# Kernel tuning notes

Measured on AMD Instinct MI355X. Metric: run time of the kernel, lower is better.

The kernel has to match this reference:

```python
import jax, jax.numpy as jnp
import numpy as np

INPUT_SIZE = 1024
HIDDEN_SIZE = 1024
NUM_LAYERS = 5
B, T = 64, 512


def setup_inputs() -> dict:
    key = jax.random.key(0)
    ks = jax.random.split(key, 12)
    scale_in = 1.0 / np.sqrt(INPUT_SIZE)
    scale_h = 1.0 / np.sqrt(HIDDEN_SIZE)
    return {
        "x": jax.random.normal(ks[0], (B, T, INPUT_SIZE), dtype=jnp.float32),
        "s0": jnp.zeros((B, HIDDEN_SIZE), dtype=jnp.float32),
        "w_h": jax.random.normal(ks[1], (INPUT_SIZE, HIDDEN_SIZE), dtype=jnp.float32) * scale_in,
        "w_t": jax.random.normal(ks[2], (INPUT_SIZE, HIDDEN_SIZE), dtype=jnp.float32) * scale_in,
        "w_c": jax.random.normal(ks[3], (INPUT_SIZE, HIDDEN_SIZE), dtype=jnp.float32) * scale_in,
        "r_hw": jax.random.normal(ks[4], (NUM_LAYERS, HIDDEN_SIZE, HIDDEN_SIZE), dtype=jnp.float32) * scale_h,
        "r_tw": jax.random.normal(ks[5], (NUM_LAYERS, HIDDEN_SIZE, HIDDEN_SIZE), dtype=jnp.float32) * scale_h,
        "r_cw": jax.random.normal(ks[6], (NUM_LAYERS, HIDDEN_SIZE, HIDDEN_SIZE), dtype=jnp.float32) * scale_h,
        "r_hb": jnp.zeros((NUM_LAYERS, HIDDEN_SIZE), dtype=jnp.float32),
        "r_tb": jnp.full((NUM_LAYERS, HIDDEN_SIZE), -1.0, dtype=jnp.float32),  # transform bias init
        "r_cb": jnp.zeros((NUM_LAYERS, HIDDEN_SIZE), dtype=jnp.float32),
    }


def reference(x, s0, w_h, w_t, w_c, r_hw, r_tw, r_cw, r_hb, r_tb, r_cb):
    # x: [B, T, D_in]; s0: [B, H]. dropout=0 -> dropout layers are identity.
    L = r_hw.shape[0]

    def step(s, x_t):
        # Input projections only feed layer 0 (l == 0 in the torch loop).
        whx = x_t @ w_h  # [B, H]
        wtx = x_t @ w_t
        wcx = x_t @ w_c
        for l in range(L):  # small fixed recurrence depth
            h_in = s @ r_hw[l] + r_hb[l]
            t_in = s @ r_tw[l] + r_tb[l]
            c_in = s @ r_cw[l] + r_cb[l]
            if l == 0:
                h_in = h_in + whx
                t_in = t_in + wtx
                c_in = c_in + wcx
            h = jnp.tanh(h_in)
            t = jax.nn.sigmoid(t_in)
            c = jax.nn.sigmoid(c_in)
            s = h * t + s * c
        return s, s

    xs = jnp.swapaxes(x, 0, 1)  # [T, B, D_in] for scan over time
    s_final, ys = jax.lax.scan(step, s0, xs)
    outputs = jnp.swapaxes(ys, 0, 1)  # [B, T, H]
    return outputs, s_final
```

## Files before the change

### kernel.cpp

```cpp
#include <hip/hip_runtime.h>

typedef _Float16 f16;
typedef f16  f16x8 __attribute__((ext_vector_type(8)));
typedef float f32x4 __attribute__((ext_vector_type(4)));
typedef unsigned int u32;
typedef unsigned long long u64;

#define NBLK   256
#define TPB    512
#define TSTEPS 512
#define NL     5
#define HDIM   1024
#define NROUND (TSTEPS*NL)
#define WSLOT  6
#define LDS_RED_OFF 147456
#define SMEM_BYTES  (147456 + 4096)

__device__ __forceinline__ float fsigmoid(float v){ return 1.0f/(1.0f + __expf(-v)); }
__device__ __forceinline__ float ftanh(float v){ return 1.0f - 2.0f/(__expf(2.0f*v) + 1.0f); }

__device__ __forceinline__ size_t frag_off_bytes(int row, int col){
    const int mt = row >> 4, pp = row & 15;
    const int kh = col >> 9, kk = (col >> 5) & 15, g8 = (col >> 3) & 3, i = col & 7;
    return (size_t)(((kh*4 + mt)*16 + kk)*1024 + (g8*16 + pp)*16 + i*2);
}

__global__ void cvt_x_kernel(const float* __restrict__ x, f16* __restrict__ xT){
    const size_t idx = (size_t)blockIdx.x*blockDim.x + threadIdx.x;
    const size_t e = idx*8;
    const int k  = (int)(e & 1023);
    const int tt = (int)((e >> 10) & 511);
    const int b  = (int)(e >> 19);
    const float4 v0 = *(const float4*)(x + e);
    const float4 v1 = *(const float4*)(x + e + 4);
    f16x8 o;
    o[0]=(f16)v0.x; o[1]=(f16)v0.y; o[2]=(f16)v0.z; o[3]=(f16)v0.w;
    o[4]=(f16)v1.x; o[5]=(f16)v1.y; o[6]=(f16)v1.z; o[7]=(f16)v1.w;
    char* dst = (char*)xT + (size_t)tt*131072 + frag_off_bytes(b, k);
    *(f16x8*)dst = o;
}

#define LOADA(i) asm volatile("global_load_dwordx4 %0, %1, off sc0 sc1" : "=v"(a##i) : "v"(ap + (i)*1024))

template<bool USE_XT>
__global__ __launch_bounds__(TPB, 2)
void rhn_persistent(const float* __restrict__ x,
                    const f16*  __restrict__ xT,
                    const float* __restrict__ s0,
                    const float* __restrict__ w_h, const float* __restrict__ w_t, const float* __restrict__ w_c,
                    const float* __restrict__ r_hw, const float* __restrict__ r_tw, const float* __restrict__ r_cw,
                    const float* __restrict__ r_hb, const float* __restrict__ r_tb, const float* __restrict__ r_cb,
                    f16* __restrict__ sb0, f16* __restrict__ sb1,
                    u32* __restrict__ flags,
                    float* __restrict__ out)
{
    extern __shared__ char smem[];
    f16*   lw  = (f16*)smem;
    f32x4* red = (f32x4*)(smem + LDS_RED_OFF);

    const int tid = threadIdx.x;
    const int ln  = tid & 63;
    const int wid = tid >> 6;
    const int mt  = wid & 3;
    const int kh  = wid >> 2;
    const int c   = blockIdx.x;
    const int g   = ln >> 4;
    const int p   = ln & 15;
    const int pe  = (p < 12) ? p : 11;
    const int gsw = (g + (pe >> 1)) & 3;

    for (int s = 0; s < WSLOT; ++s) {
        for (int mu = 0; mu < 3; ++mu) {
            const float* W;
            if (s < NL) W = (mu==0 ? r_hw : (mu==1 ? r_tw : r_cw)) + (size_t)s*HDIM*HDIM;
            else        W = (mu==0 ? w_h  : (mu==1 ? w_t  : w_c));
            for (int k = tid; k < HDIM; k += TPB) {
                const float4 v = *(const float4*)(W + (size_t)k*HDIM + 4*c);
                const int kk = k >> 5, gg = (k >> 3) & 3, ii = k & 7;
                #pragma unroll
                for (int w = 0; w < 4; ++w) {
                    const int pe2 = mu*4 + w;
                    const int gs  = (gg + (pe2 >> 1)) & 3;
                    const float val = (w==0) ? v.x : (w==1) ? v.y : (w==2) ? v.z : v.w;
                    lw[((s*32 + kk)*12 + pe2)*32 + gs*8 + ii] = (f16)val;
                }
            }
        }
    }

    const int R    = ln >> 2;
    const int jj   = ln & 3;
    const int jcol = 4*c + jj;
    const int bat  = mt*16 + R;
    const size_t sfoff = frag_off_bytes(bat, jcol & ~1);
    float s_cur = 0.f;
    float bh[NL], bt[NL], bc[NL];
    if (kh == 0) {
        s_cur = s0[(size_t)bat*HDIM + jcol];
        #pragma unroll
        for (int l = 0; l < NL; ++l) {
            bh[l] = r_hb[l*HDIM + jcol];
            bt[l] = r_tb[l*HDIM + jcol];
            bc[l] = r_cb[l*HDIM + jcol];
        }
        union { f16 h; unsigned short u; } cv; cv.h = (f16)s_cur;
        u32 mybits = cv.u;
        u32 otherbits = (u32)(unsigned short)__shfl_xor((int)mybits, 1);
        if ((jj & 1) == 0) {
            u32 packed = mybits | (otherbits << 16);
            u32* dst = (u32*)((char*)sb0 + sfoff);
            __hip_atomic_store(dst, packed, __ATOMIC_RELAXED, __HIP_MEMORY_SCOPE_AGENT);
        }
        asm volatile("s_waitcnt vmcnt(0)" ::: "memory");
    }
    __syncthreads();
    if (tid == 0)
        __hip_atomic_store(&flags[c], 1u, __ATOMIC_RELAXED, __HIP_MEMORY_SCOPE_AGENT);

    const f16* sbufs[2] = { sb0, sb1 };
    int t = 0, l = 0;
    unsigned guard = 0;

    for (int r = 0; r < NROUND; ++r) {
        const u32 tgt = (u32)(r + 1);
        if (mt == 0 && guard < (1u<<22)) {
            const u64* fp = (const u64*)&flags[kh*128 + 2*ln];
            for (;;) {
                u64 ff = __hip_atomic_load(fp, __ATOMIC_RELAXED, __HIP_MEMORY_SCOPE_AGENT);
                if (__all((u32)ff >= tgt && (u32)(ff >> 32) >= tgt)) break;
                if (++guard >= (1u<<22)) break;
                __builtin_amdgcn_s_sleep(2);
            }
        }
        __syncthreads();

        const char* ap = (const char*)sbufs[r & 1] + (size_t)((kh*4 + mt)*16)*1024 + ln*16;
        f16x8 a0,a1,a2,a3,a4,a5,a6,a7,a8,a9,a10,a11,a12,a13,a14,a15;
        LOADA(0);  LOADA(1);  LOADA(2);  LOADA(3);
        LOADA(4);  LOADA(5);  LOADA(6);  LOADA(7);
        LOADA(8);  LOADA(9);  LOADA(10); LOADA(11);
        LOADA(12); LOADA(13); LOADA(14); LOADA(15);

        f32x4 acc = {0.f,0.f,0.f,0.f};
        const f16* bp = lw + ((l*32 + kh*16)*12 + pe)*32 + gsw*8;

        if (l == 0) {
            const f16* bp5 = lw + ((5*32 + kh*16)*12 + pe)*32 + gsw*8;
            if (USE_XT) {
                const f16* xp = xT + (size_t)t*65536 + (size_t)((kh*4 + mt)*16)*512 + ln*8;
                #pragma unroll
                for (int kk = 0; kk < 16; ++kk) {
                    f16x8 xa = *(const f16x8*)(xp + kk*512);
                    f16x8 b  = *(const f16x8*)(bp5 + kk*384);
                    acc = __builtin_amdgcn_mfma_f32_16x16x32_f16(xa, b, acc, 0, 0, 0);
                }
            } else {
                const int arow = mt*16 + p;
                const float* xp = x + ((size_t)arow*TSTEPS + t)*HDIM + kh*512 + g*8;
                #pragma unroll
                for (int kk = 0; kk < 16; ++kk) {
                    float4 v0 = *(const float4*)(xp + kk*32);
                    float4 v1 = *(const float4*)(xp + kk*32 + 4);
                    f16x8 xa;
                    xa[0]=(f16)v0.x; xa[1]=(f16)v0.y; xa[2]=(f16)v0.z; xa[3]=(f16)v0.w;
                    xa[4]=(f16)v1.x; xa[5]=(f16)v1.y; xa[6]=(f16)v1.z; xa[7]=(f16)v1.w;
                    f16x8 b = *(const f16x8*)(bp5 + kk*384);
                    acc = __builtin_amdgcn_mfma_f32_16x16x32_f16(xa, b, acc, 0, 0, 0);
                }
            }
        }

        asm volatile("s_waitcnt vmcnt(0)" ::: "memory");
        __builtin_amdgcn_sched_barrier(0);
        acc = __builtin_amdgcn_mfma_f32_16x16x32_f16(a0,  *(const f16x8*)(bp + 0*384),  acc, 0,0,0);
        acc = __builtin_amdgcn_mfma_f32_16x16x32_f16(a1,  *(const f16x8*)(bp + 1*384),  acc, 0,0,0);
        acc = __builtin_amdgcn_mfma_f32_16x16x32_f16(a2,  *(const f16x8*)(bp + 2*384),  acc, 0,0,0);
        acc = __builtin_amdgcn_mfma_f32_16x16x32_f16(a3,  *(const f16x8*)(bp + 3*384),  acc, 0,0,0);
        acc = __builtin_amdgcn_mfma_f32_16x16x32_f16(a4,  *(const f16x8*)(bp + 4*384),  acc, 0,0,0);
        acc = __builtin_amdgcn_mfma_f32_16x16x32_f16(a5,  *(const f16x8*)(bp + 5*384),  acc, 0,0,0);
        acc = __builtin_amdgcn_mfma_f32_16x16x32_f16(a6,  *(const f16x8*)(bp + 6*384),  acc, 0,0,0);
        acc = __builtin_amdgcn_mfma_f32_16x16x32_f16(a7,  *(const f16x8*)(bp + 7*384),  acc, 0,0,0);
        acc = __builtin_amdgcn_mfma_f32_16x16x32_f16(a8,  *(const f16x8*)(bp + 8*384),  acc, 0,0,0);
        acc = __builtin_amdgcn_mfma_f32_16x16x32_f16(a9,  *(const f16x8*)(bp + 9*384),  acc, 0,0,0);
        acc = __builtin_amdgcn_mfma_f32_16x16x32_f16(a10, *(const f16x8*)(bp + 10*384), acc, 0,0,0);
        acc = __builtin_amdgcn_mfma_f32_16x16x32_f16(a11, *(const f16x8*)(bp + 11*384), acc, 0,0,0);
        acc = __builtin_amdgcn_mfma_f32_16x16x32_f16(a12, *(const f16x8*)(bp + 12*384), acc, 0,0,0);
        acc = __builtin_amdgcn_mfma_f32_16x16x32_f16(a13, *(const f16x8*)(bp + 13*384), acc, 0,0,0);
        acc = __builtin_amdgcn_mfma_f32_16x16x32_f16(a14, *(const f16x8*)(bp + 14*384), acc, 0,0,0);
        acc = __builtin_amdgcn_mfma_f32_16x16x32_f16(a15, *(const f16x8*)(bp + 15*384), acc, 0,0,0);

        if (kh == 1) red[mt*64 + ln] = acc;
        __syncthreads();
        if (kh == 0) {
            acc += red[mt*64 + ln];
            const int sl = (R >> 2)*16 + jj;
            const int ri = R & 3;
            float hv, tv, cv;
            { float v0=__shfl(acc[0],sl),   v1=__shfl(acc[1],sl),   v2=__shfl(acc[2],sl),   v3=__shfl(acc[3],sl);
              hv = ri==0?v0: ri==1?v1: ri==2?v2: v3; }
            { float v0=__shfl(acc[0],sl+4), v1=__shfl(acc[1],sl+4), v2=__shfl(acc[2],sl+4), v3=__shfl(acc[3],sl+4);
              tv = ri==0?v0: ri==1?v1: ri==2?v2: v3; }
            { float v0=__shfl(acc[0],sl+8), v1=__shfl(acc[1],sl+8), v2=__shfl(acc[2],sl+8), v3=__shfl(acc[3],sl+8);
              cv = ri==0?v0: ri==1?v1: ri==2?v2: v3; }
            hv += bh[l]; tv += bt[l]; cv += bc[l];
            const float hh = ftanh(hv);
            const float tg = fsigmoid(tv);
            const float cg = fsigmoid(cv);
            const float s_new = hh*tg + s_cur*cg;
            s_cur = s_new;
            f16* sbn = (f16*)sbufs[(r + 1) & 1];
            union { f16 h; unsigned short u; } cv2; cv2.h = (f16)s_new;
            u32 mybits = cv2.u;
            u32 otherbits = (u32)(unsigned short)__shfl_xor((int)mybits, 1);
            if ((jj & 1) == 0) {
                u32 packed = mybits | (otherbits << 16);
                u32* dst = (u32*)((char*)sbn + sfoff);
                __hip_atomic_store(dst, packed, __ATOMIC_RELAXED, __HIP_MEMORY_SCOPE_AGENT);
            }
            if (l == NL-1) out[((size_t)bat*TSTEPS + t)*HDIM + jcol] = s_new;
            asm volatile("s_waitcnt vmcnt(0)" ::: "memory");
        }
        __syncthreads();
        if (tid == 0)
            __hip_atomic_store(&flags[c], (u32)(r + 2), __ATOMIC_RELAXED, __HIP_MEMORY_SCOPE_AGENT);

        if (++l == NL) { l = 0; ++t; }
    }
    if (kh == 0)
        out[(size_t)64*TSTEPS*HDIM + (size_t)bat*HDIM + jcol] = s_cur;
}

extern "C" void kernel_launch(void* const* d_in, const int* in_sizes, int n_in,
                              void* d_out, int out_size, void* d_ws, size_t ws_size,
                              hipStream_t stream)
{
    const float* x    = (const float*)d_in[0];
    const float* s0   = (const float*)d_in[1];
    const float* w_h  = (const float*)d_in[2];
    const float* w_t  = (const float*)d_in[3];
    const float* w_c  = (const float*)d_in[4];
    const float* r_hw = (const float*)d_in[5];
    const float* r_tw = (const float*)d_in[6];
    const float* r_cw = (const float*)d_in[7];
    const float* r_hb = (const float*)d_in[8];
    const float* r_tb = (const float*)d_in[9];
    const float* r_cb = (const float*)d_in[10];
    float* out = (float*)d_out;

    char* ws   = (char*)d_ws;
    u32*  flags = (u32*)ws;
    f16*  sb0  = (f16*)(ws + 4096);
    f16*  sb1  = (f16*)(ws + 4096 + 131072);
    f16*  xT   = (f16*)(ws + 4096 + 262144);
    const size_t need_xt = 4096 + 262144 + (size_t)TSTEPS*64*HDIM*2;
    const bool use_xt = (ws_size >= need_xt);

    hipMemsetAsync(flags, 0, 1024, stream);
    if (use_xt)
        cvt_x_kernel<<<dim3(16384), dim3(256), 0, stream>>>(x, xT);

    hipFuncSetAttribute((const void*)rhn_persistent<true>,
                        hipFuncAttributeMaxDynamicSharedMemorySize, SMEM_BYTES);
    hipFuncSetAttribute((const void*)rhn_persistent<false>,
                        hipFuncAttributeMaxDynamicSharedMemorySize, SMEM_BYTES);

    if (use_xt)
        rhn_persistent<true><<<dim3(NBLK), dim3(TPB), SMEM_BYTES, stream>>>(
            x, xT, s0, w_h, w_t, w_c, r_hw, r_tw, r_cw, r_hb, r_tb, r_cb,
            sb0, sb1, flags, out);
    else
        rhn_persistent<false><<<dim3(NBLK), dim3(TPB), SMEM_BYTES, stream>>>(
            x, xT, s0, w_h, w_t, w_c, r_hw, r_tw, r_cw, r_hb, r_tb, r_cb,
            sb0, sb1, flags, out);
}
```

Baseline: 17.30 ms.

## Halve block size so each wave owns full K and drop intra-block barriers

The persistent kernel goes from 512 to 256 threads per block. Each wave now covers the full 1024-wide reduction with two accumulators, so the LDS cross-wave reduction and its __syncthreads disappear. Every wave polls all 256 flags itself, and a shared atomic counter lets the fourth finishing wave publish the block's flag, replacing the block barriers around the flag wait and store. The cost is twice the register pressure for the A fragments, more polling traffic per block, and a longer serial MFMA chain per wave.

```diff
diff --git a/kernel.cpp b/kernel.cpp
--- a/kernel.cpp
+++ b/kernel.cpp
@@ -7,14 +7,20 @@
 typedef unsigned long long u64;
 
 #define NBLK   256
-#define TPB    512
+#define TPB    256
 #define TSTEPS 512
 #define NL     5
 #define HDIM   1024
 #define NROUND (TSTEPS*NL)
 #define WSLOT  6
-#define LDS_RED_OFF 147456
-#define SMEM_BYTES  (147456 + 4096)
+#define GMAX   (1u<<22)
+#define SMEM_BYTES  147456
+
+#define WS_FLAGS 0
+#define WS_SB0   4096
+#define WS_SB1   (4096 + 131072)
+#define WS_XT    (4096 + 262144)
+#define WS_NEED  ((size_t)(4096 + 262144) + (size_t)TSTEPS*64*HDIM*2)
 
 __device__ __forceinline__ float fsigmoid(float v){ return 1.0f/(1.0f + __expf(-v)); }
 __device__ __forceinline__ float ftanh(float v){ return 1.0f - 2.0f/(__expf(2.0f*v) + 1.0f); }
@@ -40,10 +46,10 @@
     *(f16x8*)dst = o;
 }
 
-#define LOADA(i) asm volatile("global_load_dwordx4 %0, %1, off sc0 sc1" : "=v"(a##i) : "v"(ap + (i)*1024))
+#define LOADA(v, base, i) asm volatile("global_load_dwordx4 %0, %1, off sc0 sc1" : "=v"(v) : "v"((base) + (i)*1024))
 
 template<bool USE_XT>
-__global__ __launch_bounds__(TPB, 2)
+__global__ __launch_bounds__(TPB, 1)
 void rhn_persistent(const float* __restrict__ x,
                     const f16*  __restrict__ xT,
                     const float* __restrict__ s0,
@@ -55,14 +61,12 @@
                     float* __restrict__ out)
 {
     extern __shared__ char smem[];
-    f16*   lw  = (f16*)smem;
-    f32x4* red = (f32x4*)(smem + LDS_RED_OFF);
+    f16* lw = (f16*)smem;
+    __shared__ u32 done;
 
     const int tid = threadIdx.x;
     const int ln  = tid & 63;
-    const int wid = tid >> 6;
-    const int mt  = wid & 3;
-    const int kh  = wid >> 2;
+    const int w   = tid >> 6;
     const int c   = blockIdx.x;
     const int g   = ln >> 4;
     const int p   = ln & 15;
@@ -78,31 +82,33 @@
                 const float4 v = *(const float4*)(W + (size_t)k*HDIM + 4*c);
                 const int kk = k >> 5, gg = (k >> 3) & 3, ii = k & 7;
                 #pragma unroll
-                for (int w = 0; w < 4; ++w) {
-                    const int pe2 = mu*4 + w;
+                for (int q = 0; q < 4; ++q) {
+                    const int pe2 = mu*4 + q;
                     const int gs  = (gg + (pe2 >> 1)) & 3;
-                    const float val = (w==0) ? v.x : (w==1) ? v.y : (w==2) ? v.z : v.w;
+                    const float val = (q==0) ? v.x : (q==1) ? v.y : (q==2) ? v.z : v.w;
                     lw[((s*32 + kk)*12 + pe2)*32 + gs*8 + ii] = (f16)val;
                 }
             }
         }
     }
+
+    if (tid == 0) done = 0;
+    __syncthreads();
 
     const int R    = ln >> 2;
     const int jj   = ln & 3;
     const int jcol = 4*c + jj;
-    const int bat  = mt*16 + R;
+    const int bat  = w*16 + R;
     const size_t sfoff = frag_off_bytes(bat, jcol & ~1);
-    float s_cur = 0.f;
+    float s_cur = s0[(size_t)bat*HDIM + jcol];
     float bh[NL], bt[NL], bc[NL];
-    if (kh == 0) {
-        s_cur = s0[(size_t)bat*HDIM + jcol];
-        #pragma unroll
-        for (int l = 0; l < NL; ++l) {
-            bh[l] = r_hb[l*HDIM + jcol];
-            bt[l] = r_tb[l*HDIM + jcol];
-            bc[l] = r_cb[l*HDIM + jcol];
-        }
+    #pragma unroll
+    for (int l = 0; l < NL; ++l) {
+        bh[l] = r_hb[l*HDIM + jcol];
+        bt[l] = r_tb[l*HDIM + jcol];
+        bc[l] = r_cb[l*HDIM + jcol];
+    }
+    {
         union { f16 h; unsigned short u; } cv; cv.h = (f16)s_cur;
         u32 mybits = cv.u;
         u32 otherbits = (u32)(unsigned short)__shfl_xor((int)mybits, 1);
@@ -112,122 +118,138 @@
             __hip_atomic_store(dst, packed, __ATOMIC_RELAXED, __HIP_MEMORY_SCOPE_AGENT);
         }
         asm volatile("s_waitcnt vmcnt(0)" ::: "memory");
-    }
-    __syncthreads();
-    if (tid == 0)
-        __hip_atomic_store(&flags[c], 1u, __ATOMIC_RELAXED, __HIP_MEMORY_SCOPE_AGENT);
+        if (ln == 0) {
+            u32 old = atomicAdd(&done, 1u);
+            if ((old & 3) == 3)
+                __hip_atomic_store(&flags[c], 1u, __ATOMIC_RELAXED, __HIP_MEMORY_SCOPE_AGENT);
+        }
+    }
 
     const f16* sbufs[2] = { sb0, sb1 };
     int t = 0, l = 0;
     unsigned guard = 0;
 
     for (int r = 0; r < NROUND; ++r) {
-        const u32 tgt = (u32)(r + 1);
-        if (mt == 0 && guard < (1u<<22)) {
-            const u64* fp = (const u64*)&flags[kh*128 + 2*ln];
+        const u32 want = (u32)(r + 1);
+
+        if (guard < GMAX) {
+            const u64* fp = (const u64*)flags;
             for (;;) {
-                u64 ff = __hip_atomic_load(fp, __ATOMIC_RELAXED, __HIP_MEMORY_SCOPE_AGENT);
-                if (__all((u32)ff >= tgt && (u32)(ff >> 32) >= tgt)) break;
-                if (++guard >= (1u<<22)) break;
-                __builtin_amdgcn_s_sleep(2);
+                u64 f0 = __hip_atomic_load(fp + ln,      __ATOMIC_RELAXED, __HIP_MEMORY_SCOPE_AGENT);
+                u64 f1 = __hip_atomic_load(fp + 64 + ln, __ATOMIC_RELAXED, __HIP_MEMORY_SCOPE_AGENT);
+                bool ok = (u32)f0 >= want && (u32)(f0 >> 32) >= want &&
+                          (u32)f1 >= want && (u32)(f1 >> 32) >= want;
+                if (__all(ok)) break;
+                if (++guard >= GMAX) break;
+                __builtin_amdgcn_s_sleep(1);
             }
         }
-        __syncthreads();
-
-        const char* ap = (const char*)sbufs[r & 1] + (size_t)((kh*4 + mt)*16)*1024 + ln*16;
+
+        const char* ap0 = (const char*)sbufs[r & 1] + (size_t)(w*16)*1024       + ln*16;
+        const char* ap1 = (const char*)sbufs[r & 1] + (size_t)((4 + w)*16)*1024 + ln*16;
         f16x8 a0,a1,a2,a3,a4,a5,a6,a7,a8,a9,a10,a11,a12,a13,a14,a15;
-        LOADA(0);  LOADA(1);  LOADA(2);  LOADA(3);
-        LOADA(4);  LOADA(5);  LOADA(6);  LOADA(7);
-        LOADA(8);  LOADA(9);  LOADA(10); LOADA(11);
-        LOADA(12); LOADA(13); LOADA(14); LOADA(15);
-
-        f32x4 acc = {0.f,0.f,0.f,0.f};
-        const f16* bp = lw + ((l*32 + kh*16)*12 + pe)*32 + gsw*8;
+        f16x8 a16,a17,a18,a19,a20,a21,a22,a23,a24,a25,a26,a27,a28,a29,a30,a31;
+        LOADA(a0 ,ap0,0);  LOADA(a1 ,ap0,1);  LOADA(a2 ,ap0,2);  LOADA(a3 ,ap0,3);
+        LOADA(a4 ,ap0,4);  LOADA(a5 ,ap0,5);  LOADA(a6 ,ap0,6);  LOADA(a7 ,ap0,7);
+        LOADA(a8 ,ap0,8);  LOADA(a9 ,ap0,9);  LOADA(a10,ap0,10); LOADA(a11,ap0,11);
+        LOADA(a12,ap0,12); LOADA(a13,ap0,13); LOADA(a14,ap0,14); LOADA(a15,ap0,15);
+        LOADA(a16,ap1,0);  LOADA(a17,ap1,1);  LOADA(a18,ap1,2);  LOADA(a19,ap1,3);
+        LOADA(a20,ap1,4);  LOADA(a21,ap1,5);  LOADA(a22,ap1,6);  LOADA(a23,ap1,7);
+        LOADA(a24,ap1,8);  LOADA(a25,ap1,9);  LOADA(a26,ap1,10); LOADA(a27,ap1,11);
+        LOADA(a28,ap1,12); LOADA(a29,ap1,13); LOADA(a30,ap1,14); LOADA(a31,ap1,15);
+
+        f32x4 acc0 = {0.f,0.f,0.f,0.f};
+        f32x4 acc1 = {0.f,0.f,0.f,0.f};
+        const f16* bp = lw + (size_t)((l*32)*12 + pe)*32 + gsw*8;
 
         if (l == 0) {
-            const f16* bp5 = lw + ((5*32 + kh*16)*12 + pe)*32 + gsw*8;
+            const f16* bp5 = lw + (size_t)((5*32)*12 + pe)*32 + gsw*8;
             if (USE_XT) {
-                const f16* xp = xT + (size_t)t*65536 + (size_t)((kh*4 + mt)*16)*512 + ln*8;
+                const f16* xp0 = xT + (size_t)t*65536 + (size_t)(w*16)*512       + ln*8;
+                const f16* xp1 = xT + (size_t)t*65536 + (size_t)((4 + w)*16)*512 + ln*8;
                 #pragma unroll
                 for (int kk = 0; kk < 16; ++kk) {
-                    f16x8 xa = *(const f16x8*)(xp + kk*512);
-                    f16x8 b  = *(const f16x8*)(bp5 + kk*384);
-                    acc = __builtin_amdgcn_mfma_f32_16x16x32_f16(xa, b, acc, 0, 0, 0);
+                    f16x8 xa = *(const f16x8*)(xp0 + kk*512);
+                    acc0 = __builtin_amdgcn_mfma_f32_16x16x32_f16(xa, *(const f16x8*)(bp5 + kk*384), acc0, 0,0,0);
+                }
+                #pragma unroll
+                for (int kk = 0; kk < 16; ++kk) {
+                    f16x8 xa = *(const f16x8*)(xp1 + kk*512);
+                    acc1 = __builtin_amdgcn_mfma_f32_16x16x32_f16(xa, *(const f16x8*)(bp5 + (16 + kk)*384), acc1, 0,0,0);
                 }
             } else {
-                const int arow = mt*16 + p;
-                const float* xp = x + ((size_t)arow*TSTEPS + t)*HDIM + kh*512 + g*8;
-                #pragma unroll
-                for (int kk = 0; kk < 16; ++kk) {
-                    float4 v0 = *(const float4*)(xp + kk*32);
-                    float4 v1 = *(const float4*)(xp + kk*32 + 4);
+                const int arow = w*16 + p;
+                const float* xp = x + ((size_t)arow*TSTEPS + t)*HDIM + g*8;
+                #pragma unroll
+                for (int kidx = 0; kidx < 32; ++kidx) {
+                    float4 v0 = *(const float4*)(xp + kidx*32);
+                    float4 v1 = *(const float4*)(xp + kidx*32 + 4);
                     f16x8 xa;
                     xa[0]=(f16)v0.x; xa[1]=(f16)v0.y; xa[2]=(f16)v0.z; xa[3]=(f16)v0.w;
                     xa[4]=(f16)v1.x; xa[5]=(f16)v1.y; xa[6]=(f16)v1.z; xa[7]=(f16)v1.w;
-                    f16x8 b = *(const f16x8*)(bp5 + kk*384);
-                    acc = __builtin_amdgcn_mfma_f32_16x16x32_f16(xa, b, acc, 0, 0, 0);
+                    if (kidx & 1)
+                        acc1 = __builtin_amdgcn_mfma_f32_16x16x32_f16(xa, *(const f16x8*)(bp5 + kidx*384), acc1, 0,0,0);
+                    else
+                        acc0 = __builtin_amdgcn_mfma_f32_16x16x32_f16(xa, *(const f16x8*)(bp5 + kidx*384), acc0, 0,0,0);
                 }
             }
         }
 
         asm volatile("s_waitcnt vmcnt(0)" ::: "memory");
         __builtin_amdgcn_sched_barrier(0);
-        acc = __builtin_amdgcn_mfma_f32_16x16x32_f16(a0,  *(const f16x8*)(bp + 0*384),  acc, 0,0,0);
-        acc = __builtin_amdgcn_mfma_f32_16x16x32_f16(a1,  *(const f16x8*)(bp + 1*384),  acc, 0,0,0);
-        acc = __builtin_amdgcn_mfma_f32_16x16x32_f16(a2,  *(const f16x8*)(bp + 2*384),  acc, 0,0,0);
-        acc = __builtin_amdgcn_mfma_f32_16x16x32_f16(a3,  *(const f16x8*)(bp + 3*384),  acc, 0,0,0);
-        acc = __builtin_amdgcn_mfma_f32_16x16x32_f16(a4,  *(const f16x8*)(bp + 4*384),  acc, 0,0,0);
-        acc = __builtin_amdgcn_mfma_f32_16x16x32_f16(a5,  *(const f16x8*)(bp + 5*384),  acc, 0,0,0);
-        acc = __builtin_amdgcn_mfma_f32_16x16x32_f16(a6,  *(const f16x8*)(bp + 6*384),  acc, 0,0,0);
-        acc = __builtin_amdgcn_mfma_f32_16x16x32_f16(a7,  *(const f16x8*)(bp + 7*384),  acc, 0,0,0);
-        acc = __builtin_amdgcn_mfma_f32_16x16x32_f16(a8,  *(const f16x8*)(bp + 8*384),  acc, 0,0,0);
-        acc = __builtin_amdgcn_mfma_f32_16x16x32_f16(a9,  *(const f16x8*)(bp + 9*384),  acc, 0,0,0);
-        acc = __builtin_amdgcn_mfma_f32_16x16x32_f16(a10, *(const f16x8*)(bp + 10*384), acc, 0,0,0);
-        acc = __builtin_amdgcn_mfma_f32_16x16x32_f16(a11, *(const f16x8*)(bp + 11*384), acc, 0,0,0);
-        acc = __builtin_amdgcn_mfma_f32_16x16x32_f16(a12, *(const f16x8*)(bp + 12*384), acc, 0,0,0);
-        acc = __builtin_amdgcn_mfma_f32_16x16x32_f16(a13, *(const f16x8*)(bp + 13*384), acc, 0,0,0);
-        acc = __builtin_amdgcn_mfma_f32_16x16x32_f16(a14, *(const f16x8*)(bp + 14*384), acc, 0,0,0);
-        acc = __builtin_amdgcn_mfma_f32_16x16x32_f16(a15, *(const f16x8*)(bp + 15*384), acc, 0,0,0);
-
-        if (kh == 1) red[mt*64 + ln] = acc;
-        __syncthreads();
-        if (kh == 0) {
-            acc += red[mt*64 + ln];
-            const int sl = (R >> 2)*16 + jj;
-            const int ri = R & 3;
-            float hv, tv, cv;
-            { float v0=__shfl(acc[0],sl),   v1=__shfl(acc[1],sl),   v2=__shfl(acc[2],sl),   v3=__shfl(acc[3],sl);
-              hv = ri==0?v0: ri==1?v1: ri==2?v2: v3; }
-            { float v0=__shfl(acc[0],sl+4), v1=__shfl(acc[1],sl+4), v2=__shfl(acc[2],sl+4), v3=__shfl(acc[3],sl+4);
-              tv = ri==0?v0: ri==1?v1: ri==2?v2: v3; }
-            { float v0=__shfl(acc[0],sl+8), v1=__shfl(acc[1],sl+8), v2=__shfl(acc[2],sl+8), v3=__shfl(acc[3],sl+8);
-              cv = ri==0?v0: ri==1?v1: ri==2?v2: v3; }
-            hv += bh[l]; tv += bt[l]; cv += bc[l];
-            const float hh = ftanh(hv);
-            const float tg = fsigmoid(tv);
-            const float cg = fsigmoid(cv);
-            const float s_new = hh*tg + s_cur*cg;
-            s_cur = s_new;
-            f16* sbn = (f16*)sbufs[(r + 1) & 1];
-            union { f16 h; unsigned short u; } cv2; cv2.h = (f16)s_new;
-            u32 mybits = cv2.u;
-            u32 otherbits = (u32)(unsigned short)__shfl_xor((int)mybits, 1);
-            if ((jj & 1) == 0) {
-                u32 packed = mybits | (otherbits << 16);
-                u32* dst = (u32*)((char*)sbn + sfoff);
-                __hip_atomic_store(dst, packed, __ATOMIC_RELAXED, __HIP_MEMORY_SCOPE_AGENT);
-            }
-            if (l == NL-1) out[((size_t)bat*TSTEPS + t)*HDIM + jcol] = s_new;
-            asm volatile("s_waitcnt vmcnt(0)" ::: "memory");
-        }
-        __syncthreads();
-        if (tid == 0)
-            __hip_atomic_store(&flags[c], (u32)(r + 2), __ATOMIC_RELAXED, __HIP_MEMORY_SCOPE_AGENT);
+        #define AMF(i, v) do { \
+            if ((i) & 1) acc1 = __builtin_amdgcn_mfma_f32_16x16x32_f16(v, *(const f16x8*)(bp + (i)*384), acc1, 0,0,0); \
+            else         acc0 = __builtin_amdgcn_mfma_f32_16x16x32_f16(v, *(const f16x8*)(bp + (i)*384), acc0, 0,0,0); \
+        } while(0)
+        AMF(0,a0);  AMF(1,a1);  AMF(2,a2);  AMF(3,a3);
+        AMF(4,a4);  AMF(5,a5);  AMF(6,a6);  AMF(7,a7);
+        AMF(8,a8);  AMF(9,a9);  AMF(10,a10); AMF(11,a11);
+        AMF(12,a12); AMF(13,a13); AMF(14,a14); AMF(15,a15);
+        AMF(16,a16); AMF(17,a17); AMF(18,a18); AMF(19,a19);
+        AMF(20,a20); AMF(21,a21); AMF(22,a22); AMF(23,a23);
+        AMF(24,a24); AMF(25,a25); AMF(26,a26); AMF(27,a27);
+        AMF(28,a28); AMF(29,a29); AMF(30,a30); AMF(31,a31);
+        #undef AMF
+
+        f32x4 acc = acc0 + acc1;
+
+        const int sl = (R >> 2)*16 + jj;
+        const int ri = R & 3;
+        float hv, tv, cv;
+        { float v0=__shfl(acc[0],sl),   v1=__shfl(acc[1],sl),   v2=__shfl(acc[2],sl),   v3=__shfl(acc[3],sl);
+          hv = ri==0?v0: ri==1?v1: ri==2?v2: v3; }
+        { float v0=__shfl(acc[0],sl+4), v1=__shfl(acc[1],sl+4), v2=__shfl(acc[2],sl+4), v3=__shfl(acc[3],sl+4);
+          tv = ri==0?v0: ri==1?v1: ri==2?v2: v3; }
+        { float v0=__shfl(acc[0],sl+8), v1=__shfl(acc[1],sl+8), v2=__shfl(acc[2],sl+8), v3=__shfl(acc[3],sl+8);
+          cv = ri==0?v0: ri==1?v1: ri==2?v2: v3; }
+        hv += bh[l]; tv += bt[l]; cv += bc[l];
+        const float hh = ftanh(hv);
+        const float tg = fsigmoid(tv);
+        const float cg = fsigmoid(cv);
+        const float s_new = hh*tg + s_cur*cg;
+        s_cur = s_new;
+
+        f16* sbn = (f16*)sbufs[(r + 1) & 1];
+        union { f16 h; unsigned short u; } cv2; cv2.h = (f16)s_new;
+        u32 mybits = cv2.u;
+        u32 otherbits = (u32)(unsigned short)__shfl_xor((int)mybits, 1);
+        if ((jj & 1) == 0) {
+            u32 packed = mybits | (otherbits << 16);
+            u32* dst = (u32*)((char*)sbn + sfoff);
+            __hip_atomic_store(dst, packed, __ATOMIC_RELAXED, __HIP_MEMORY_SCOPE_AGENT);
+        }
+        if (l == NL-1) out[((size_t)bat*TSTEPS + t)*HDIM + jcol] = s_new;
+        asm volatile("s_waitcnt vmcnt(0)" ::: "memory");
+
+        if (ln == 0) {
+            u32 old = atomicAdd(&done, 1u);
+            if ((old & 3) == 3)
+                __hip_atomic_store(&flags[c], (u32)(r + 2), __ATOMIC_RELAXED, __HIP_MEMORY_SCOPE_AGENT);
+        }
 
         if (++l == NL) { l = 0; ++t; }
     }
-    if (kh == 0)
-        out[(size_t)64*TSTEPS*HDIM + (size_t)bat*HDIM + jcol] = s_cur;
+    out[(size_t)64*TSTEPS*HDIM + (size_t)bat*HDIM + jcol] = s_cur;
 }
 
 extern "C" void kernel_launch(void* const* d_in, const int* in_sizes, int n_in,
@@ -247,15 +269,14 @@
     const float* r_cb = (const float*)d_in[10];
     float* out = (float*)d_out;
 
-    char* ws   = (char*)d_ws;
-    u32*  flags = (u32*)ws;
-    f16*  sb0  = (f16*)(ws + 4096);
-    f16*  sb1  = (f16*)(ws + 4096 + 131072);
-    f16*  xT   = (f16*)(ws + 4096 + 262144);
-    const size_t need_xt = 4096 + 262144 + (size_t)TSTEPS*64*HDIM*2;
-    const bool use_xt = (ws_size >= need_xt);
-
-    hipMemsetAsync(flags, 0, 1024, stream);
+    char* ws    = (char*)d_ws;
+    u32*  flags = (u32*)(ws + WS_FLAGS);
+    f16*  sb0   = (f16*)(ws + WS_SB0);
+    f16*  sb1   = (f16*)(ws + WS_SB1);
+    f16*  xT    = (f16*)(ws + WS_XT);
+    const bool use_xt = (ws_size >= WS_NEED);
+
+    hipMemsetAsync(flags, 0, 4096, stream);
     if (use_xt)
         cvt_x_kernel<<<dim3(16384), dim3(256), 0, stream>>>(x, xT);
 
```

Result: slower. 28.48 ms (+64.7%).

## Replace per-round block barriers with per-wave flag polling and LDS completion counter

Applied to the files above, without the earlier changes.

Every wave now polls all 256 block flags itself instead of one wave polling and then a block-wide barrier. The reduction buffer is double-buffered by round parity, which removes the trailing __syncthreads. The block flag is published by whichever of the four kh==0 waves finishes last, tracked with an LDS atomic counter. This cuts two block barriers per round from the serial recurrence, at the cost of more global flag traffic (8 waves polling without sleep) and subtler ordering guarantees between waves.

```diff
diff --git a/kernel.cpp b/kernel.cpp
--- a/kernel.cpp
+++ b/kernel.cpp
@@ -13,8 +13,9 @@
 #define HDIM   1024
 #define NROUND (TSTEPS*NL)
 #define WSLOT  6
+#define GMAX   (1u<<22)
 #define LDS_RED_OFF 147456
-#define SMEM_BYTES  (147456 + 4096)
+#define SMEM_BYTES  (147456 + 8192)
 
 __device__ __forceinline__ float fsigmoid(float v){ return 1.0f/(1.0f + __expf(-v)); }
 __device__ __forceinline__ float ftanh(float v){ return 1.0f - 2.0f/(__expf(2.0f*v) + 1.0f); }
@@ -57,6 +58,7 @@
     extern __shared__ char smem[];
     f16*   lw  = (f16*)smem;
     f32x4* red = (f32x4*)(smem + LDS_RED_OFF);
+    __shared__ u32 done;
 
     const int tid = threadIdx.x;
     const int ln  = tid & 63;
@@ -87,6 +89,7 @@
             }
         }
     }
+    if (tid == 0) done = 0;
 
     const int R    = ln >> 2;
     const int jj   = ln & 3;
@@ -122,17 +125,19 @@
     unsigned guard = 0;
 
     for (int r = 0; r < NROUND; ++r) {
-        const u32 tgt = (u32)(r + 1);
-        if (mt == 0 && guard < (1u<<22)) {
-            const u64* fp = (const u64*)&flags[kh*128 + 2*ln];
+        const u32 want = (u32)(r + 1);
+
+        if (guard < GMAX) {
+            const u64* fp = (const u64*)flags;
             for (;;) {
-                u64 ff = __hip_atomic_load(fp, __ATOMIC_RELAXED, __HIP_MEMORY_SCOPE_AGENT);
-                if (__all((u32)ff >= tgt && (u32)(ff >> 32) >= tgt)) break;
-                if (++guard >= (1u<<22)) break;
-                __builtin_amdgcn_s_sleep(2);
-            }
-        }
-        __syncthreads();
+                u64 f0 = __hip_atomic_load(fp + ln,      __ATOMIC_RELAXED, __HIP_MEMORY_SCOPE_AGENT);
+                u64 f1 = __hip_atomic_load(fp + 64 + ln, __ATOMIC_RELAXED, __HIP_MEMORY_SCOPE_AGENT);
+                bool ok = (u32)f0 >= want && (u32)(f0 >> 32) >= want &&
+                          (u32)f1 >= want && (u32)(f1 >> 32) >= want;
+                if (__all(ok)) break;
+                if (++guard >= GMAX) break;
+            }
+        }
 
         const char* ap = (const char*)sbufs[r & 1] + (size_t)((kh*4 + mt)*16)*1024 + ln*16;
         f16x8 a0,a1,a2,a3,a4,a5,a6,a7,a8,a9,a10,a11,a12,a13,a14,a15;
@@ -189,10 +194,10 @@
         acc = __builtin_amdgcn_mfma_f32_16x16x32_f16(a14, *(const f16x8*)(bp + 14*384), acc, 0,0,0);
         acc = __builtin_amdgcn_mfma_f32_16x16x32_f16(a15, *(const f16x8*)(bp + 15*384), acc, 0,0,0);
 
-        if (kh == 1) red[mt*64 + ln] = acc;
+        if (kh == 1) red[(r & 1)*256 + mt*64 + ln] = acc;
         __syncthreads();
         if (kh == 0) {
-            acc += red[mt*64 + ln];
+            acc += red[(r & 1)*256 + mt*64 + ln];
             const int sl = (R >> 2)*16 + jj;
             const int ri = R & 3;
             float hv, tv, cv;
@@ -219,10 +224,12 @@
             }
             if (l == NL-1) out[((size_t)bat*TSTEPS + t)*HDIM + jcol] = s_new;
             asm volatile("s_waitcnt vmcnt(0)" ::: "memory");
-        }
-        __syncthreads();
-        if (tid == 0)
-            __hip_atomic_store(&flags[c], (u32)(r + 2), __ATOMIC_RELAXED, __HIP_MEMORY_SCOPE_AGENT);
+            if (ln == 0) {
+                u32 old = atomicAdd(&done, 1u);
+                if ((old & 3) == 3)
+                    __hip_atomic_store(&flags[c], (u32)(r + 2), __ATOMIC_RELAXED, __HIP_MEMORY_SCOPE_AGENT);
+            }
+        }
 
         if (++l == NL) { l = 0; ++t; }
     }
```

Measured after the change: 30.94 ms. +78.9%, slower.
